# Kernel optimization log

Measured on AMD Instinct MI355X. Metric: run time of the kernel, lower is better.

## Reference

```python
import jax, jax.numpy as jnp
import numpy as np

CIN, COUT, K = 64, 64, 3
ALPHA = 8.3
STRIDE, PAD, DIL = 1, 1, 1
B, H = 8, 128


def _unfold(x, k, dilation, padding, stride):
    # torch.nn.functional.unfold: output feature order is (C, kh, kw)
    x = jnp.pad(x, ((0, 0), (0, 0), (padding, padding), (padding, padding)))
    b, c, h, w = x.shape
    eff = dilation * (k - 1) + 1
    oh = (h - eff) // stride + 1
    ow = (w - eff) // stride + 1
    cols = []
    for i in range(k):
        for j in range(k):
            cols.append(x[:, :, i * dilation:i * dilation + stride * oh:stride,
                              j * dilation:j * dilation + stride * ow:stride])
    p = jnp.stack(cols, axis=2)          # [B, C, k*k, oh, ow]
    return p.reshape(b, c * k * k, oh * ow)


def setup_inputs() -> dict:
    key = jax.random.key(0)
    k1, k2, k3, k4 = jax.random.split(key, 4)
    image = jax.random.normal(k1, (B, CIN, H, H), dtype=jnp.float32)
    depth = jax.random.uniform(k2, (B, 1, H, H), dtype=jnp.float32)
    weight = jax.random.normal(k3, (COUT, CIN, K, K), dtype=jnp.float32) * 0.05
    bias = jax.random.normal(k4, (COUT,), dtype=jnp.float32) * 0.05
    return {"image": image, "depth": depth, "weight": weight, "bias": bias}


def reference(image, depth, weight, bias):
    # im2col of the image: [B, L, Cin*k*k]
    patches = _unfold(image, K, DIL, PAD, STRIDE).transpose(0, 2, 1)
    b, L, _ = patches.shape
    # depth is repeat()'d to Cin channels in the original; the unfolded depth
    # columns therefore tile the single-channel patch Cin times. Exploit that:
    dpatch = _unfold(depth, K, DIL, PAD, STRIDE).transpose(0, 2, 1)  # [B, L, k*k]
    # original centre index: int((Cin*k*k)/2); within the tiled patch this is
    # position (Cin*k*k//2) % (k*k) of the single-channel patch
    centre_idx = (CIN * K * K // 2) % (K * K)
    centre = dpatch[:, :, centre_idx:centre_idx + 1]
    sim = jnp.exp(-ALPHA * jnp.abs(dpatch - centre))  # [B, L, k*k]
    # modulate per kernel offset (broadcast over channels == tiled similarity)
    modulated = patches.reshape(b, L, CIN, K * K) * sim[:, :, None, :]
    out = jnp.einsum('blck,ock->blo', modulated, weight.reshape(COUT, CIN, K * K))
    out = out + bias
    osz = (image.shape[-1] + 2 * PAD - DIL * (K - 1) - 1) // STRIDE + 1
    return out.transpose(0, 2, 1).reshape(b, COUT, osz, osz)
```

## Files before the change

### kernel.cpp

```cpp
#include <hip/hip_runtime.h>
#include <hip/hip_bf16.h>

#define BATCH 8
#define CIN   64
#define COUT  64
#define HH    128
#define WW    128
#define HW    (HH * WW)
#define ALPHA 8.3f
#define TPX   64
#define YPB   2
#define XW    66

typedef __attribute__((ext_vector_type(8))) short short8;
typedef __attribute__((ext_vector_type(4))) float f32x4;

__device__ __forceinline__ int img_idx(int r, int x, int c) {
    return (((r * XW + x) << 6) + c) ^ ((x & 7) << 3);
}

__global__ __launch_bounds__(256)
void depthconv_fused(const float* __restrict__ image,
                     const float* __restrict__ depth,
                     const float* __restrict__ weight,
                     const float* __restrict__ bias,
                     float* __restrict__ out) {
    __shared__ short s_img[4 * XW * 64];
    __shared__ float s_d[4][XW];
    __shared__ float s_sim[YPB][9][TPX];

    const int tid = threadIdx.x;
    const int bid = blockIdx.x;
    const int yg = bid & 63;
    const int xt = (bid >> 6) & 1;
    const int b  = bid >> 7;
    const int x0 = xt * TPX;
    const int y0 = yg * YPB;

    const int lane = tid & 63;
    const int wid  = tid >> 6;
    const int l15  = lane & 15;
    const int lq   = lane >> 4;
    const int o_base = wid * 16;

    short8 wfrag[9][2];
    {
        const int o = o_base + l15;
        #pragma unroll
        for (int h = 0; h < 2; ++h) {
            const float* wp = &weight[(o * CIN + h * 32 + lq * 8) * 9];
            #pragma unroll
            for (int q4 = 0; q4 < 18; ++q4) {
                float4 f = *(const float4*)&wp[q4 * 4];
                #pragma unroll
                for (int e = 0; e < 4; ++e) {
                    const int q  = q4 * 4 + e;
                    const int cj = q / 9, tap = q % 9;
                    const float fe = (e == 0) ? f.x : (e == 1) ? f.y : (e == 2) ? f.z : f.w;
                    wfrag[tap][h][cj] =
                        __builtin_bit_cast(short, __float2bfloat16(fe));
                }
            }
        }
    }

    float bias_v[4];
    #pragma unroll
    for (int r = 0; r < 4; ++r) bias_v[r] = bias[o_base + lq * 4 + r];

    {
        const int sx  = 1 + (tid & 63);
        const int srr = tid >> 6;
        const int gy  = y0 - 1 + srr;
        const int gx  = x0 + (tid & 63);
        const bool yok = (unsigned)gy < HH;
        const float* ip = &image[((b * CIN) * HH + gy) * WW + gx];
        const int base = (srr * XW + sx) << 6;
        const int swz  = (sx & 7) << 3;
        #pragma unroll 8
        for (int c2 = 0; c2 < 32; ++c2) {
            float v0 = 0.f, v1 = 0.f;
            if (yok) { v0 = ip[0]; v1 = ip[HW]; }
            ip += 2 * HW;
            __hip_bfloat162 pk = __float22bfloat162_rn(float2{v0, v1});
            *(__hip_bfloat162*)&s_img[base + ((2 * c2) ^ swz)] = pk;
        }
    }
    {
        const int e   = tid & 1;
        const int sx  = e ? (XW - 1) : 0;
        const int rr  = (tid >> 1) & 3;
        const int c2  = tid >> 3;
        const int gy  = y0 - 1 + rr;
        const int gx  = x0 - 1 + sx;
        float v0 = 0.f, v1 = 0.f;
        if ((unsigned)gy < HH && (unsigned)gx < WW) {
            const float* p = &image[((b * CIN + 2 * c2) * HH + gy) * WW + gx];
            v0 = p[0]; v1 = p[HW];
        }
        __hip_bfloat162 pk = __float22bfloat162_rn(float2{v0, v1});
        *(__hip_bfloat162*)&s_img[img_idx(rr, sx, 2 * c2)] = pk;
    }
    for (int i = tid; i < 4 * XW; i += 256) {
        int rr = i / XW, x = i - rr * XW;
        int gy = y0 - 1 + rr, gx = x0 - 1 + x;
        float v = 0.f;
        if ((unsigned)gy < HH && (unsigned)gx < WW)
            v = depth[(b * HH + gy) * WW + gx];
        s_d[rr][x] = v;
    }
    __syncthreads();

    for (int i = tid; i < YPB * 9 * TPX; i += 256) {
        int p  = i & 63;
        int t  = i >> 6;
        int yy = t / 9, tap = t - yy * 9;
        int ri = tap / 3, dj = tap - ri * 3;
        float dt = s_d[yy + ri][p + dj];
        float dc = s_d[yy][p];
        s_sim[yy][tap][p] = __expf(-ALPHA * fabsf(dt - dc));
    }
    __syncthreads();

    for (int yy = 0; yy < YPB; ++yy) {
        f32x4 acc[4];
        #pragma unroll
        for (int nt = 0; nt < 4; ++nt) acc[nt] = f32x4{0.f, 0.f, 0.f, 0.f};

        #pragma unroll
        for (int tap = 0; tap < 9; ++tap) {
            const int ri = tap / 3, dj = tap % 3;
            #pragma unroll
            for (int nt = 0; nt < 4; ++nt) {
                const int xi = nt * 16 + l15 + dj;
                short8 b0 = *(const short8*)&s_img[img_idx(yy + ri, xi, lq * 8)];
                f32x4 tmp = __builtin_amdgcn_mfma_f32_16x16x32_bf16(
                    wfrag[tap][0], b0, (f32x4){0.f, 0.f, 0.f, 0.f}, 0, 0, 0);
                short8 b1 = *(const short8*)&s_img[img_idx(yy + ri, xi, 32 + lq * 8)];
                tmp = __builtin_amdgcn_mfma_f32_16x16x32_bf16(
                    wfrag[tap][1], b1, tmp, 0, 0, 0);
                const float sv = s_sim[yy][tap][nt * 16 + l15];
                #pragma unroll
                for (int r = 0; r < 4; ++r)
                    acc[nt][r] = fmaf(sv, tmp[r], acc[nt][r]);
            }
        }

        const int y = y0 + yy;
        #pragma unroll
        for (int nt = 0; nt < 4; ++nt) {
            const int px = x0 + nt * 16 + l15;
            #pragma unroll
            for (int r = 0; r < 4; ++r) {
                const int o = o_base + lq * 4 + r;
                out[((b * COUT + o) * HH + y) * WW + px] = acc[nt][r] + bias_v[r];
            }
        }
    }
}

extern "C" void kernel_launch(void* const* d_in, const int* in_sizes, int n_in,
                              void* d_out, int out_size, void* d_ws, size_t ws_size,
                              hipStream_t stream) {
    const float* image  = (const float*)d_in[0];
    const float* depth  = (const float*)d_in[1];
    const float* weight = (const float*)d_in[2];
    const float* bias   = (const float*)d_in[3];
    float* out = (float*)d_out;

    dim3 grid(BATCH * (HH / YPB) * (WW / TPX));
    depthconv_fused<<<grid, 256, 0, stream>>>(image, depth, weight, bias, out);
}
```

Measured before the change: 130.9 us.

## Pre-transpose weights to bf16 and reuse LDS image rows across output rows

Result: faster. 121.5 us (-7.2%).

```diff
diff --git a/kernel.cpp b/kernel.cpp
--- a/kernel.cpp
+++ b/kernel.cpp
@@ -20,10 +20,20 @@
 }
 
 __global__ __launch_bounds__(256)
+void transpose_w(const float* __restrict__ w, __hip_bfloat16* __restrict__ wt) {
+    int i = blockIdx.x * 256 + threadIdx.x;
+    if (i >= 9 * 64 * 64) return;
+    int c = i & 63;
+    int o = (i >> 6) & 63;
+    int tap = i >> 12;
+    wt[i] = __float2bfloat16(w[(o * 64 + c) * 9 + tap]);
+}
+
+__global__ __launch_bounds__(256)
 void depthconv_fused(const float* __restrict__ image,
                      const float* __restrict__ depth,
-                     const float* __restrict__ weight,
                      const float* __restrict__ bias,
+                     const short* __restrict__ wt,
                      float* __restrict__ out) {
     __shared__ short s_img[4 * XW * 64];
     __shared__ float s_d[4][XW];
@@ -44,25 +54,11 @@
     const int o_base = wid * 16;
 
     short8 wfrag[9][2];
-    {
-        const int o = o_base + l15;
+    #pragma unroll
+    for (int tap = 0; tap < 9; ++tap)
         #pragma unroll
-        for (int h = 0; h < 2; ++h) {
-            const float* wp = &weight[(o * CIN + h * 32 + lq * 8) * 9];
-            #pragma unroll
-            for (int q4 = 0; q4 < 18; ++q4) {
-                float4 f = *(const float4*)&wp[q4 * 4];
-                #pragma unroll
-                for (int e = 0; e < 4; ++e) {
-                    const int q  = q4 * 4 + e;
-                    const int cj = q / 9, tap = q % 9;
-                    const float fe = (e == 0) ? f.x : (e == 1) ? f.y : (e == 2) ? f.z : f.w;
-                    wfrag[tap][h][cj] =
-                        __builtin_bit_cast(short, __float2bfloat16(fe));
-                }
-            }
-        }
-    }
+        for (int h = 0; h < 2; ++h)
+            wfrag[tap][h] = *(const short8*)&wt[(tap * 64 + o_base + l15) * 64 + h * 32 + lq * 8];
 
     float bias_v[4];
     #pragma unroll
@@ -77,7 +73,7 @@
         const float* ip = &image[((b * CIN) * HH + gy) * WW + gx];
         const int base = (srr * XW + sx) << 6;
         const int swz  = (sx & 7) << 3;
-        #pragma unroll 8
+        #pragma unroll 16
         for (int c2 = 0; c2 < 32; ++c2) {
             float v0 = 0.f, v1 = 0.f;
             if (yok) { v0 = ip[0]; v1 = ip[HW]; }
@@ -122,39 +118,54 @@
     }
     __syncthreads();
 
-    for (int yy = 0; yy < YPB; ++yy) {
-        f32x4 acc[4];
-        #pragma unroll
-        for (int nt = 0; nt < 4; ++nt) acc[nt] = f32x4{0.f, 0.f, 0.f, 0.f};
+    #pragma unroll
+    for (int nt = 0; nt < 4; ++nt) {
+        const int xb = nt * 16 + l15;
+        f32x4 a0 = f32x4{0.f, 0.f, 0.f, 0.f};
+        f32x4 a1 = f32x4{0.f, 0.f, 0.f, 0.f};
 
         #pragma unroll
-        for (int tap = 0; tap < 9; ++tap) {
-            const int ri = tap / 3, dj = tap % 3;
+        for (int r = 0; r < 4; ++r) {
+            short8 bb[3][2];
             #pragma unroll
-            for (int nt = 0; nt < 4; ++nt) {
-                const int xi = nt * 16 + l15 + dj;
-                short8 b0 = *(const short8*)&s_img[img_idx(yy + ri, xi, lq * 8)];
-                f32x4 tmp = __builtin_amdgcn_mfma_f32_16x16x32_bf16(
-                    wfrag[tap][0], b0, (f32x4){0.f, 0.f, 0.f, 0.f}, 0, 0, 0);
-                short8 b1 = *(const short8*)&s_img[img_idx(yy + ri, xi, 32 + lq * 8)];
-                tmp = __builtin_amdgcn_mfma_f32_16x16x32_bf16(
-                    wfrag[tap][1], b1, tmp, 0, 0, 0);
-                const float sv = s_sim[yy][tap][nt * 16 + l15];
+            for (int dj = 0; dj < 3; ++dj) {
+                bb[dj][0] = *(const short8*)&s_img[img_idx(r, xb + dj, lq * 8)];
+                bb[dj][1] = *(const short8*)&s_img[img_idx(r, xb + dj, 32 + lq * 8)];
+            }
+            if (r < 3) {
                 #pragma unroll
-                for (int r = 0; r < 4; ++r)
-                    acc[nt][r] = fmaf(sv, tmp[r], acc[nt][r]);
+                for (int dj = 0; dj < 3; ++dj) {
+                    const int tap = 3 * r + dj;
+                    f32x4 tmp = __builtin_amdgcn_mfma_f32_16x16x32_bf16(
+                        wfrag[tap][0], bb[dj][0], (f32x4){0.f, 0.f, 0.f, 0.f}, 0, 0, 0);
+                    tmp = __builtin_amdgcn_mfma_f32_16x16x32_bf16(
+                        wfrag[tap][1], bb[dj][1], tmp, 0, 0, 0);
+                    const float sv = s_sim[0][tap][xb];
+                    #pragma unroll
+                    for (int e = 0; e < 4; ++e) a0[e] = fmaf(sv, tmp[e], a0[e]);
+                }
+            }
+            if (r >= 1) {
+                #pragma unroll
+                for (int dj = 0; dj < 3; ++dj) {
+                    const int tap = 3 * (r - 1) + dj;
+                    f32x4 tmp = __builtin_amdgcn_mfma_f32_16x16x32_bf16(
+                        wfrag[tap][0], bb[dj][0], (f32x4){0.f, 0.f, 0.f, 0.f}, 0, 0, 0);
+                    tmp = __builtin_amdgcn_mfma_f32_16x16x32_bf16(
+                        wfrag[tap][1], bb[dj][1], tmp, 0, 0, 0);
+                    const float sv = s_sim[1][tap][xb];
+                    #pragma unroll
+                    for (int e = 0; e < 4; ++e) a1[e] = fmaf(sv, tmp[e], a1[e]);
+                }
             }
         }
 
-        const int y = y0 + yy;
+        const int px = x0 + xb;
         #pragma unroll
-        for (int nt = 0; nt < 4; ++nt) {
-            const int px = x0 + nt * 16 + l15;
-            #pragma unroll
-            for (int r = 0; r < 4; ++r) {
-                const int o = o_base + lq * 4 + r;
-                out[((b * COUT + o) * HH + y) * WW + px] = acc[nt][r] + bias_v[r];
-            }
+        for (int rr = 0; rr < 4; ++rr) {
+            const int o = o_base + lq * 4 + rr;
+            out[((b * COUT + o) * HH + y0) * WW + px]     = a0[rr] + bias_v[rr];
+            out[((b * COUT + o) * HH + y0 + 1) * WW + px] = a1[rr] + bias_v[rr];
         }
     }
 }
@@ -167,7 +178,11 @@
     const float* weight = (const float*)d_in[2];
     const float* bias   = (const float*)d_in[3];
     float* out = (float*)d_out;
+    __hip_bfloat16* wt = (__hip_bfloat16*)d_ws;
+
+    transpose_w<<<(9 * 64 * 64 + 255) / 256, 256, 0, stream>>>(weight, wt);
 
     dim3 grid(BATCH * (HH / YPB) * (WW / TPX));
-    depthconv_fused<<<grid, 256, 0, stream>>>(image, depth, weight, bias, out);
+    depthconv_fused<<<grid, 256, 0, stream>>>(image, depth, bias,
+                                              (const short*)wt, out);
 }
```
